# Kernel optimization log

Hardware: AMD Instinct MI355X
Metric: run time of the kernel (lower is better)

Reference implementation:

```python
import jax, jax.numpy as jnp
import numpy as np
import math

V = 32000      # vocab_size
D = 1024       # hidden_dims
T_MAX = 1024   # max_txt_len
L = 4          # n_layers
H = 8          # heads (fixed in CausalMHA)
HD = D // H
B, T = 2, 1024
EPS = 1e-5


def setup_inputs() -> dict:
    key = jax.random.key(0)
    ks = jax.random.split(key, 20)
    s = 0.02
    inp = {
        "x": jax.random.randint(ks[0], (B, T), 0, V, dtype=jnp.int64) if jax.config.read("jax_enable_x64") else jax.random.randint(ks[0], (B, T), 0, V, dtype=jnp.int32),
        "tok_emb": jax.random.normal(ks[1], (V, D), jnp.float32) * s,
        "pos_emb": jax.random.normal(ks[2], (1, T_MAX, D), jnp.float32) * s,
        "ln1_g": jnp.ones((L, D), jnp.float32),
        "ln1_b": jnp.zeros((L, D), jnp.float32),
        "wqkv": jax.random.normal(ks[3], (L, D, 3 * D), jnp.float32) * s,
        "bqkv": jnp.zeros((L, 3 * D), jnp.float32),
        "wo": jax.random.normal(ks[4], (L, D, D), jnp.float32) * s,
        "bo": jnp.zeros((L, D), jnp.float32),
        "ln2_g": jnp.ones((L, D), jnp.float32),
        "ln2_b": jnp.zeros((L, D), jnp.float32),
        "wfc": jax.random.normal(ks[5], (L, D, 4 * D), jnp.float32) * s,   # no bias
        "wfc2": jax.random.normal(ks[6], (L, 4 * D, D), jnp.float32) * s,  # no bias
        "fn_g": jnp.ones((D,), jnp.float32),
        "fn_b": jnp.zeros((D,), jnp.float32),
        "wout": jax.random.normal(ks[7], (D, V), jnp.float32) * s,
        "bout": jnp.zeros((V,), jnp.float32),
    }
    return inp


def _ln(x, g, b):
    mu = jnp.mean(x, axis=-1, keepdims=True)
    var = jnp.var(x, axis=-1, keepdims=True)
    return (x - mu) * jax.lax.rsqrt(var + EPS) * g + b


def _attn(xn, wqkv_l, bqkv_l, wo_l, bo_l):
    Bb, Tt, _ = xn.shape
    qkv = xn @ wqkv_l + bqkv_l                      # [B,T,3D]
    q, k, v = jnp.split(qkv, 3, axis=-1)
    q = q.reshape(Bb, Tt, H, HD)
    k = k.reshape(Bb, Tt, H, HD)
    v = v.reshape(Bb, Tt, H, HD)
    scores = jnp.einsum("bqhd,bkhd->bhqk", q, k) / math.sqrt(HD)
    mask = jnp.triu(jnp.ones((Tt, Tt), bool), k=1)   # True above diagonal
    scores = jnp.where(mask, jnp.float32(-jnp.inf), scores)
    att = jax.nn.softmax(scores, axis=-1)
    out = jnp.einsum("bhqk,bkhd->bqhd", att, v).reshape(Bb, Tt, D)
    return out @ wo_l + bo_l


def reference(x, tok_emb, pos_emb, ln1_g, ln1_b, wqkv, bqkv, wo, bo,
              ln2_g, ln2_b, wfc, wfc2, fn_g, fn_b, wout, bout):
    Tt = x.shape[1]
    h = tok_emb[x] + pos_emb[:, :Tt, :]              # [B,T,D]
    for i in range(L):
        h = h + _attn(_ln(h, ln1_g[i], ln1_b[i]), wqkv[i], bqkv[i], wo[i], bo[i])
        hn = _ln(h, ln2_g[i], ln2_b[i])
        h = h + jax.nn.gelu(hn @ wfc[i], approximate=False) @ wfc2[i]
    h = _ln(h, fn_g, fn_b)
    return h @ wout + bout                           # [B,T,V] logits
```

## Files before the change

kernel.cpp:

```cpp
#include <hip/hip_runtime.h>
#include <math.h>
#include <stdint.h>

#define D_  1024
#define T_  1024
#define H_  8
#define HD_ 128
#define L_  4
#define V_  32000
#define M_  2048

typedef __attribute__((ext_vector_type(4))) float f32x4;
typedef __attribute__((ext_vector_type(4))) short s16x4;
typedef __attribute__((ext_vector_type(8))) short s16x8;
typedef unsigned short u16;

__device__ __forceinline__ u16 f2bf(float f) {
  union { float f; uint32_t u; } c; c.f = f;
  uint32_t r = c.u + 0x7fffu + ((c.u >> 16) & 1u);
  return (u16)(r >> 16);
}
__device__ __forceinline__ float bf2f(u16 h) {
  union { uint32_t u; float f; } c; c.u = ((uint32_t)h) << 16;
  return c.f;
}
__device__ __forceinline__ float gelu_f(float x) {
  return 0.5f * x * (1.0f + erff(x * 0.70710678118654752f));
}

__device__ __forceinline__ void gload16(const u16* g, u16* l) {
  __builtin_amdgcn_global_load_lds(
      (const __attribute__((address_space(1))) void*)(uintptr_t)g,
      (__attribute__((address_space(3))) void*)(uint32_t)(uintptr_t)l,
      16, 0, 0);
}

template<int INF32>
__global__ __launch_bounds__(256)
void convT_kernel(const void* __restrict__ inv, u16* __restrict__ out,
                  int ldin, int ldout, long inZ, long outZ)
{
  __shared__ __align__(16) u16 tile[64][72];
  const int c0 = blockIdx.x << 6, r0 = blockIdx.y << 6;
  const int t = threadIdx.x;
  const int rr = t >> 2, cs = (t & 3) << 4;
  u16 tmp[16];
  if (INF32) {
    const float* in = (const float*)inv + (size_t)blockIdx.z * inZ;
    const float* p = in + (size_t)(r0 + rr) * ldin + c0 + cs;
#pragma unroll
    for (int q = 0; q < 4; ++q) {
      f32x4 v = *(const f32x4*)(p + q * 4);
#pragma unroll
      for (int j = 0; j < 4; ++j) tmp[q * 4 + j] = f2bf(v[j]);
    }
  } else {
    const u16* in = (const u16*)inv + (size_t)blockIdx.z * inZ;
    const u16* p = in + (size_t)(r0 + rr) * ldin + c0 + cs;
    s16x8 v0 = *(const s16x8*)(p);
    s16x8 v1 = *(const s16x8*)(p + 8);
#pragma unroll
    for (int j = 0; j < 8; ++j) { tmp[j] = (u16)v0[j]; tmp[8 + j] = (u16)v1[j]; }
  }
  *(s16x8*)&tile[rr][cs]     = *(const s16x8*)tmp;
  *(s16x8*)&tile[rr][cs + 8] = *(const s16x8*)(tmp + 8);
  __syncthreads();
  const int cr = t >> 2, rs = (t & 3) << 4;
  u16 o[16];
#pragma unroll
  for (int j = 0; j < 16; ++j) o[j] = tile[rs + j][cr];
  u16* op = out + (size_t)blockIdx.z * outZ + (size_t)(c0 + cr) * ldout + r0 + rs;
  *(s16x8*)op       = *(const s16x8*)o;
  *(s16x8*)(op + 8) = *(const s16x8*)(o + 8);
}

template<int TM, int ACT, int BIAS, int OUT>
__global__ __launch_bounds__(256)
void gemm2(const u16* __restrict__ A, const u16* __restrict__ Bw,
           const float* __restrict__ bias, const float* __restrict__ res,
           void* __restrict__ Cv,
           int K, int lda, int ldb, int ldc, float scale)
{
  static_assert(TM == 64 || TM == 128, "tile");
  constexpr int WN  = (TM == 128) ? 2 : 4;
  constexpr int WNW = 128 / WN;
  constexpr int NJ  = WNW / 16;
  constexpr int AR  = TM / 64;

  const int gx = gridDim.x, gy = gridDim.y;
  int flat = blockIdx.y * gx + blockIdx.x;
  const int nwg = gx * gy;
  int swz = (flat & 7) * (nwg >> 3) + (flat >> 3);
  const int bx = swz % gx;
  const int by = swz / gx;

  const int m0 = bx * TM, n0 = by * 128;
  const int ktiles = K >> 5;

  __shared__ __align__(16) u16 As[2][TM * 32];
  __shared__ __align__(16) u16 Bs[2][128 * 32];

  const int tid = threadIdx.x, lane = tid & 63, wave = tid >> 6;
  const int wm = wave / WN, wn = wave % WN;
  const int l15 = lane & 15, l4 = lane >> 4;
  const int srow = lane >> 2, scol = (lane & 3) << 3;

  f32x4 acc[4][NJ];
  const f32x4 z4 = {0.f, 0.f, 0.f, 0.f};
#pragma unroll
  for (int i = 0; i < 4; ++i)
#pragma unroll
    for (int j = 0; j < NJ; ++j) acc[i][j] = z4;

  auto stage = [&](int kt, int buf) {
    const int kc = (kt << 5) + scol;
#pragma unroll
    for (int r = 0; r < AR; ++r) {
      const int row = r * 64 + wave * 16;
      gload16(A + (size_t)(m0 + row + srow) * lda + kc, &As[buf][row * 32]);
    }
#pragma unroll
    for (int r = 0; r < 2; ++r) {
      const int row = r * 64 + wave * 16;
      gload16(Bw + (size_t)(n0 + row + srow) * ldb + kc, &Bs[buf][row * 32]);
    }
  };

  stage(0, 0);
  __syncthreads();

  for (int kt = 0; kt < ktiles; ++kt) {
    const int buf = kt & 1;
    if (kt + 1 < ktiles) stage(kt + 1, buf ^ 1);
    const u16* ap = &As[buf][(wm * 64 + l15) * 32 + (l4 << 3)];
    const u16* bp = &Bs[buf][(wn * WNW + l15) * 32 + (l4 << 3)];
    s16x8 af[4], bf[NJ];
#pragma unroll
    for (int i = 0; i < 4; ++i) af[i] = *(const s16x8*)(ap + i * (16 * 32));
#pragma unroll
    for (int j = 0; j < NJ; ++j) bf[j] = *(const s16x8*)(bp + j * (16 * 32));
#pragma unroll
    for (int i = 0; i < 4; ++i)
#pragma unroll
      for (int j = 0; j < NJ; ++j)
        acc[i][j] = __builtin_amdgcn_mfma_f32_16x16x32_bf16(af[i], bf[j], acc[i][j], 0, 0, 0);
    __syncthreads();
  }

  float* Cf = (float*)Cv;
  u16*   Ch = (u16*)Cv;
#pragma unroll
  for (int i = 0; i < 4; ++i) {
    const int row0 = m0 + wm * 64 + i * 16 + l4 * 4;
#pragma unroll
    for (int j = 0; j < NJ; ++j) {
      const int col = n0 + wn * WNW + j * 16 + l15;
      const float bv = BIAS ? bias[col] : 0.0f;
#pragma unroll
      for (int r = 0; r < 4; ++r) {
        float v = acc[i][j][r] * scale + bv;
        if (ACT) v = gelu_f(v);
        const size_t idx = (size_t)(row0 + r) * ldc + col;
        if (OUT == 0)      Ch[idx] = f2bf(v);
        else if (OUT == 1) Cf[idx] = v;
        else               Cf[idx] = v + res[idx];
      }
    }
  }
}

__global__ __launch_bounds__(256)
void flash_attn(const u16* __restrict__ qkv, const u16* __restrict__ Vt,
                u16* __restrict__ xo)
{
  const int qb = 15 - blockIdx.x;
  const int z  = blockIdx.y;
  const int b  = z >> 3, hh = z & 7;

  __shared__ __align__(16) u16 Ks[64 * 128];
  __shared__ __align__(16) u16 Vs[128 * 64];
  __shared__ __align__(16) u16 Ps[64 * 80];

  const int tid = threadIdx.x, lane = tid & 63, w = tid >> 6;
  const int l15 = lane & 15, l4 = lane >> 4;
  const float iscale = 0.08838834764831845f;

  const int qrow = qb * 64 + w * 16 + l15;
  const u16* qptr = qkv + ((size_t)(b * T_) + qrow) * (3 * D_) + hh * HD_;

  s16x8 bQ[4];
#pragma unroll
  for (int ks = 0; ks < 4; ++ks)
    bQ[ks] = *(const s16x8*)(qptr + ks * 32 + l4 * 8);

  f32x4 O[8];
#pragma unroll
  for (int i = 0; i < 8; ++i) O[i] = {0.f, 0.f, 0.f, 0.f};
  float m_run = -1e30f, l_run = 0.f;

  const int ntiles = qb + 1;
  for (int kt = 0; kt < ntiles; ++kt) {
    __syncthreads();
    {
      const int r = tid >> 2, c = (tid & 3) << 5;
      const u16* src = qkv + ((size_t)(b * T_) + kt * 64 + r) * (3 * D_) + D_ + hh * HD_ + c;
#pragma unroll
      for (int u = 0; u < 4; ++u) {
        s16x8 v = *(const s16x8*)(src + u * 8);
        const int dblk = (c >> 3) + u;
        *(s16x8*)&Ks[r * 128 + ((dblk ^ (r & 7)) << 3)] = v;
      }
      const int d = tid >> 1, kc0 = (tid & 1) << 5;
      const u16* vsrc = Vt + ((size_t)z * HD_ + d) * T_ + kt * 64 + kc0;
#pragma unroll
      for (int u = 0; u < 4; ++u) {
        s16x8 v = *(const s16x8*)(vsrc + u * 8);
        const int kblk = (kc0 >> 3) + u;
        *(s16x8*)&Vs[d * 64 + ((kblk ^ (d & 7)) << 3)] = v;
      }
    }
    __syncthreads();

    f32x4 st[4];
#pragma unroll
    for (int mf = 0; mf < 4; ++mf) st[mf] = {0.f, 0.f, 0.f, 0.f};
#pragma unroll
    for (int ks = 0; ks < 4; ++ks) {
      s16x8 aK[4];
#pragma unroll
      for (int mf = 0; mf < 4; ++mf) {
        const int r = mf * 16 + l15;
        aK[mf] = *(const s16x8*)&Ks[r * 128 + ((((ks << 2) + l4) ^ (r & 7)) << 3)];
      }
#pragma unroll
      for (int mf = 0; mf < 4; ++mf)
        st[mf] = __builtin_amdgcn_mfma_f32_16x16x32_bf16(aK[mf], bQ[ks], st[mf], 0, 0, 0);
    }

    const bool diag = (kt == qb);
    float sv[16];
    float mx = -1e30f;
#pragma unroll
    for (int mf = 0; mf < 4; ++mf)
#pragma unroll
      for (int r = 0; r < 4; ++r) {
        float s = st[mf][r] * iscale;
        if (diag) {
          const int k = kt * 64 + mf * 16 + l4 * 4 + r;
          if (k > qrow) s = -1e30f;
        }
        sv[mf * 4 + r] = s;
        mx = fmaxf(mx, s);
      }
    mx = fmaxf(mx, __shfl_xor(mx, 16));
    mx = fmaxf(mx, __shfl_xor(mx, 32));
    const float m_new = fmaxf(m_run, mx);
    const float sc_old = __expf(m_run - m_new);
    float psum = 0.f;
    u16 pb[16];
#pragma unroll
    for (int j = 0; j < 16; ++j) {
      const float p = __expf(sv[j] - m_new);
      psum += p;
      pb[j] = f2bf(p);
    }
    psum += __shfl_xor(psum, 16);
    psum += __shfl_xor(psum, 32);
    l_run = l_run * sc_old + psum;
    m_run = m_new;

    float scr[4];
#pragma unroll
    for (int r = 0; r < 4; ++r) scr[r] = __shfl(sc_old, l4 * 4 + r);
#pragma unroll
    for (int df = 0; df < 8; ++df)
#pragma unroll
      for (int r = 0; r < 4; ++r) O[df][r] *= scr[r];

    {
      const int row = w * 16 + l15;
#pragma unroll
      for (int j = 0; j < 16; ++j) {
        const int k = (j >> 2) * 16 + l4 * 4 + (j & 3);
        Ps[row * 80 + (((k >> 3) ^ (l15 & 7)) << 3) + (k & 7)] = pb[j];
      }
    }

#pragma unroll
    for (int kc = 0; kc < 2; ++kc) {
      const int prow = w * 16 + l15;
      s16x8 aP = *(const s16x8*)&Ps[prow * 80 + ((((kc << 2) + l4) ^ (l15 & 7)) << 3)];
#pragma unroll
      for (int df = 0; df < 8; ++df) {
        const int d = df * 16 + l15;
        s16x8 bV = *(const s16x8*)&Vs[d * 64 + ((((kc << 2) + l4) ^ (d & 7)) << 3)];
        O[df] = __builtin_amdgcn_mfma_f32_16x16x32_bf16(aP, bV, O[df], 0, 0, 0);
      }
    }
  }

  const float inv_l = 1.0f / l_run;
  float invr[4];
#pragma unroll
  for (int r = 0; r < 4; ++r) invr[r] = __shfl(inv_l, l4 * 4 + r);
#pragma unroll
  for (int df = 0; df < 8; ++df)
#pragma unroll
    for (int r = 0; r < 4; ++r) {
      const int row = qb * 64 + w * 16 + l4 * 4 + r;
      xo[((size_t)(b * T_) + row) * D_ + hh * HD_ + df * 16 + l15] =
          f2bf(O[df][r] * invr[r]);
    }
}

__global__ __launch_bounds__(512, 2)
void gemm8_logits(const u16* __restrict__ A, const u16* __restrict__ Bw,
                  const float* __restrict__ bias, float* __restrict__ C)
{
  int flat = blockIdx.x;
  int swz = (flat & 7) * 125 + (flat >> 3);
  const int bx = swz & 7;
  const int by = swz >> 3;
  const int m0 = bx << 8, n0 = by << 8;

  __shared__ __align__(16) u16 lds[65536];

  const int tid = threadIdx.x, lane = tid & 63, wave = tid >> 6;
  const int wm = wave >> 2, wn = wave & 3;
  const int l15 = lane & 15, l4 = lane >> 4;

  f32x4 acc[8][4];
  const f32x4 z4 = {0.f, 0.f, 0.f, 0.f};
#pragma unroll
  for (int i = 0; i < 8; ++i)
#pragma unroll
    for (int j = 0; j < 4; ++j) acc[i][j] = z4;

  auto stg = [&](const u16* G, int rowbase, int slot, int kt, int kh) {
    if (kt >= 16) return;
#pragma unroll
    for (int r = 0; r < 2; ++r) {
      const int u = r * 512 + (wave << 6) + lane;
      const int rw = u >> 2, ks = u & 3;
      const int ksw = ks ^ ((rw >> 1) & 3);
      const u16* src = G + (size_t)(rowbase + rw) * 1024 + (kt << 6) + (kh << 5) + (ksw << 3);
      gload16(src, &lds[slot + r * 4096 + (wave << 9)]);
    }
  };

  s16x8 af[4], bfr[4];

#define LDA4(bb, kk, mh)                                                      \
  {                                                                           \
    _Pragma("unroll") for (int f = 0; f < 4; ++f) {                           \
      const int rw = wm * 128 + (mh) * 64 + f * 16 + l15;                     \
      af[f] = *(const s16x8*)&lds[(bb) + (kk) * 8192 + rw * 32 +              \
                                  ((l4 ^ ((rw >> 1) & 3)) << 3)];             \
    }                                                                         \
  }
#define LDB4(bb, kk)                                                          \
  {                                                                           \
    _Pragma("unroll") for (int f = 0; f < 4; ++f) {                           \
      const int rn = wn * 64 + f * 16 + l15;                                  \
      bfr[f] = *(const s16x8*)&lds[(bb) + 16384 + (kk) * 8192 + rn * 32 +     \
                                   ((l4 ^ ((rn >> 1) & 3)) << 3)];            \
    }                                                                         \
  }
#define MFMA16(mh)                                                            \
  {                                                                           \
    __builtin_amdgcn_s_barrier();                                             \
    asm volatile("s_waitcnt lgkmcnt(0)" ::: "memory");                        \
    __builtin_amdgcn_sched_barrier(0);                                        \
    __builtin_amdgcn_s_setprio(1);                                            \
    _Pragma("unroll") for (int f = 0; f < 4; ++f)                             \
      _Pragma("unroll") for (int nf = 0; nf < 4; ++nf)                        \
        acc[(mh) * 4 + f][nf] = __builtin_amdgcn_mfma_f32_16x16x32_bf16(      \
            af[f], bfr[nf], acc[(mh) * 4 + f][nf], 0, 0, 0);                  \
    __builtin_amdgcn_s_setprio(0);                                            \
  }
#define BAR() __builtin_amdgcn_s_barrier()
#define VM4() asm volatile("s_waitcnt vmcnt(4)" ::: "memory")

  stg(A,  m0, 0,             0, 0);
  stg(Bw, n0, 16384,         0, 0);
  stg(A,  m0, 8192,          0, 1);
  stg(Bw, n0, 16384 + 8192,  0, 1);
  stg(A,  m0, 32768,         1, 0);
  stg(Bw, n0, 32768 + 16384, 1, 0);
  VM4();
  BAR();

  for (int i = 0; i < 8; ++i) {
    const int t = 2 * i;
    LDA4(0, 0, 0); LDB4(0, 0);
    stg(A, m0, 32768 + 8192, t + 1, 1);
    MFMA16(0); BAR();
    LDA4(0, 0, 1);
    stg(Bw, n0, 32768 + 24576, t + 1, 1);
    MFMA16(1); BAR();
    LDA4(0, 1, 0); LDB4(0, 1);
    stg(A, m0, 0, t + 2, 0);
    MFMA16(0); BAR();
    LDA4(0, 1, 1);
    stg(Bw, n0, 16384, t + 2, 0);
    MFMA16(1); VM4(); BAR();
    LDA4(32768, 0, 0); LDB4(32768, 0);
    stg(A, m0, 8192, t + 2, 1);
    MFMA16(0); BAR();
    LDA4(32768, 0, 1);
    stg(Bw, n0, 16384 + 8192, t + 2, 1);
    MFMA16(1); BAR();
    LDA4(32768, 1, 0); LDB4(32768, 1);
    stg(A, m0, 32768, t + 3, 0);
    MFMA16(0); BAR();
    LDA4(32768, 1, 1);
    stg(Bw, n0, 32768 + 16384, t + 3, 0);
    MFMA16(1); VM4(); BAR();
  }
#undef LDA4
#undef LDB4
#undef MFMA16
#undef BAR
#undef VM4

  float bv[4];
#pragma unroll
  for (int nf = 0; nf < 4; ++nf) bv[nf] = bias[n0 + wn * 64 + nf * 16 + l15];
#pragma unroll
  for (int mf = 0; mf < 8; ++mf) {
    const int row0 = m0 + wm * 128 + mf * 16 + l4 * 4;
#pragma unroll
    for (int nf = 0; nf < 4; ++nf) {
      const int col = n0 + wn * 64 + nf * 16 + l15;
#pragma unroll
      for (int r = 0; r < 4; ++r)
        C[(size_t)(row0 + r) * V_ + col] = acc[mf][nf][r] + bv[nf];
    }
  }
}

__global__ __launch_bounds__(256)
void ln_bf16(const float* __restrict__ x, const float* __restrict__ g,
             const float* __restrict__ b, u16* __restrict__ y)
{
  __shared__ float red[8];
  const int row = blockIdx.x, tid = threadIdx.x;
  f32x4 v = *(const f32x4*)&x[(size_t)row * D_ + tid * 4];
  float s  = v[0] + v[1] + v[2] + v[3];
  float s2 = v[0]*v[0] + v[1]*v[1] + v[2]*v[2] + v[3]*v[3];
#pragma unroll
  for (int off = 32; off > 0; off >>= 1) {
    s  += __shfl_xor(s, off);
    s2 += __shfl_xor(s2, off);
  }
  if ((tid & 63) == 0) { red[tid >> 6] = s; red[4 + (tid >> 6)] = s2; }
  __syncthreads();
  s  = red[0] + red[1] + red[2] + red[3];
  s2 = red[4] + red[5] + red[6] + red[7];
  const float mean = s * (1.0f / D_);
  const float var  = s2 * (1.0f / D_) - mean * mean;
  const float rs   = rsqrtf(var + 1e-5f);
  f32x4 gg = *(const f32x4*)&g[tid * 4];
  f32x4 bb = *(const f32x4*)&b[tid * 4];
  u16 o[4];
#pragma unroll
  for (int j = 0; j < 4; ++j) o[j] = f2bf((v[j] - mean) * rs * gg[j] + bb[j]);
  *(s16x4*)&y[(size_t)row * D_ + tid * 4] = *(const s16x4*)o;
}

__global__ __launch_bounds__(256)
void embed_kernel(const int* __restrict__ x, const float* __restrict__ tok,
                  const float* __restrict__ pos, float* __restrict__ h)
{
  const int row = blockIdx.x, tid = threadIdx.x;
  const int t = row & (T_ - 1);
  const int id = x[row];
  f32x4 a = *(const f32x4*)&tok[(size_t)id * D_ + tid * 4];
  f32x4 p = *(const f32x4*)&pos[(size_t)t * D_ + tid * 4];
  f32x4 o = {a[0] + p[0], a[1] + p[1], a[2] + p[2], a[3] + p[3]};
  *(f32x4*)&h[(size_t)row * D_ + tid * 4] = o;
}

extern "C" void kernel_launch(void* const* d_in, const int* in_sizes, int n_in,
                              void* d_out, int out_size, void* d_ws, size_t ws_size,
                              hipStream_t stream)
{
  (void)in_sizes; (void)n_in; (void)out_size; (void)ws_size;
  const int*   x     = (const int*)  d_in[0];
  const float* tok   = (const float*)d_in[1];
  const float* pos   = (const float*)d_in[2];
  const float* ln1_g = (const float*)d_in[3];
  const float* ln1_b = (const float*)d_in[4];
  const float* wqkv  = (const float*)d_in[5];
  const float* bqkv  = (const float*)d_in[6];
  const float* wo    = (const float*)d_in[7];
  const float* bo    = (const float*)d_in[8];
  const float* ln2_g = (const float*)d_in[9];
  const float* ln2_b = (const float*)d_in[10];
  const float* wfc   = (const float*)d_in[11];
  const float* wfc2  = (const float*)d_in[12];
  const float* fn_g  = (const float*)d_in[13];
  const float* fn_b  = (const float*)d_in[14];
  const float* wout  = (const float*)d_in[15];
  const float* bout  = (const float*)d_in[16];
  float* out = (float*)d_out;

  float* h  = (float*)d_ws;
  u16* xn   = (u16*)(h + (size_t)M_ * D_);
  u16* Wq   = xn  + (size_t)M_ * D_;
  u16* Wo   = Wq  + (size_t)3 * D_ * D_;
  u16* Wf1  = Wo  + (size_t)D_ * D_;
  u16* Wf2  = Wf1 + (size_t)4 * D_ * D_;
  u16* qkv  = Wf2 + (size_t)4 * D_ * D_;
  u16* Vt   = qkv + (size_t)M_ * 3 * D_;
  u16* S    = Vt  + (size_t)2 * T_ * D_;
  u16* WoutT = Wq;

  embed_kernel<<<M_, 256, 0, stream>>>(x, tok, pos, h);

  for (int l = 0; l < L_; ++l) {
    convT_kernel<1><<<dim3(48, 16, 1), 256, 0, stream>>>(
        wqkv + (size_t)l * D_ * 3 * D_, Wq, 3 * D_, D_, 0, 0);
    convT_kernel<1><<<dim3(16, 16, 1), 256, 0, stream>>>(
        wo + (size_t)l * D_ * D_, Wo, D_, D_, 0, 0);
    convT_kernel<1><<<dim3(64, 16, 1), 256, 0, stream>>>(
        wfc + (size_t)l * D_ * 4 * D_, Wf1, 4 * D_, D_, 0, 0);
    convT_kernel<1><<<dim3(16, 64, 1), 256, 0, stream>>>(
        wfc2 + (size_t)l * 4 * D_ * D_, Wf2, D_, 4 * D_, 0, 0);

    ln_bf16<<<M_, 256, 0, stream>>>(h, ln1_g + l * D_, ln1_b + l * D_, xn);
    gemm2<128, 0, 1, 0><<<dim3(16, 24), 256, 0, stream>>>(
        xn, Wq, bqkv + l * 3 * D_, nullptr, qkv, D_, D_, D_, 3 * D_, 1.0f);
    convT_kernel<0><<<dim3(16, 16, 2), 256, 0, stream>>>(
        qkv + 2 * D_, Vt, 3 * D_, T_, (long)T_ * 3 * D_, (long)T_ * D_);
    flash_attn<<<dim3(16, 16), 256, 0, stream>>>(qkv, Vt, xn);
    gemm2<64, 0, 1, 2><<<dim3(32, 8), 256, 0, stream>>>(
        xn, Wo, bo + l * D_, h, h, D_, D_, D_, D_, 1.0f);
    ln_bf16<<<M_, 256, 0, stream>>>(h, ln2_g + l * D_, ln2_b + l * D_, xn);
    gemm2<128, 1, 0, 0><<<dim3(16, 32), 256, 0, stream>>>(
        xn, Wf1, nullptr, nullptr, S, D_, D_, D_, 4 * D_, 1.0f);
    gemm2<64, 0, 0, 2><<<dim3(32, 8), 256, 0, stream>>>(
        S, Wf2, nullptr, h, h, 4 * D_, 4 * D_, 4 * D_, D_, 1.0f);
  }

  ln_bf16<<<M_, 256, 0, stream>>>(h, fn_g, fn_b, xn);
  convT_kernel<1><<<dim3(500, 16, 1), 256, 0, stream>>>(
      wout, WoutT, V_, D_, 0, 0);
  gemm8_logits<<<1000, 512, 0, stream>>>(xn, WoutT, bout, out);
}
```

Baseline: 1.004 ms.

## Route QKV and FC1 GEMMs through 256x256 tile kernel; fuse weight conversions

Generalizes the large-tile 512-thread logits GEMM kernel with templated output type, GELU and optional bias, then uses it for the QKV and FC1 projections instead of the 128x128 gemm2 kernel. It also merges the four per-layer weight transpose/convert launches into a single 3072-block kernel. The larger tiles raise data reuse, and the merged conversion cuts launch count. The risk is that the big-tile grids are small (96 and 128 blocks), which may leave many compute units idle on a 256-CU part.

```diff
diff --git a/kernel.cpp b/kernel.cpp
--- a/kernel.cpp
+++ b/kernel.cpp
@@ -35,32 +35,21 @@
       16, 0, 0);
 }
 
-template<int INF32>
-__global__ __launch_bounds__(256)
-void convT_kernel(const void* __restrict__ inv, u16* __restrict__ out,
-                  int ldin, int ldout, long inZ, long outZ)
-{
-  __shared__ __align__(16) u16 tile[64][72];
-  const int c0 = blockIdx.x << 6, r0 = blockIdx.y << 6;
+__device__ __forceinline__ void convT_f32_tile(const float* __restrict__ in,
+                                               u16* __restrict__ out,
+                                               int ldin, int ldout,
+                                               int c0, int r0,
+                                               u16 (*tile)[72])
+{
   const int t = threadIdx.x;
   const int rr = t >> 2, cs = (t & 3) << 4;
   u16 tmp[16];
-  if (INF32) {
-    const float* in = (const float*)inv + (size_t)blockIdx.z * inZ;
-    const float* p = in + (size_t)(r0 + rr) * ldin + c0 + cs;
-#pragma unroll
-    for (int q = 0; q < 4; ++q) {
-      f32x4 v = *(const f32x4*)(p + q * 4);
-#pragma unroll
-      for (int j = 0; j < 4; ++j) tmp[q * 4 + j] = f2bf(v[j]);
-    }
-  } else {
-    const u16* in = (const u16*)inv + (size_t)blockIdx.z * inZ;
-    const u16* p = in + (size_t)(r0 + rr) * ldin + c0 + cs;
-    s16x8 v0 = *(const s16x8*)(p);
-    s16x8 v1 = *(const s16x8*)(p + 8);
-#pragma unroll
-    for (int j = 0; j < 8; ++j) { tmp[j] = (u16)v0[j]; tmp[8 + j] = (u16)v1[j]; }
+  const float* p = in + (size_t)(r0 + rr) * ldin + c0 + cs;
+#pragma unroll
+  for (int q = 0; q < 4; ++q) {
+    f32x4 v = *(const f32x4*)(p + q * 4);
+#pragma unroll
+    for (int j = 0; j < 4; ++j) tmp[q * 4 + j] = f2bf(v[j]);
   }
   *(s16x8*)&tile[rr][cs]     = *(const s16x8*)tmp;
   *(s16x8*)&tile[rr][cs + 8] = *(const s16x8*)(tmp + 8);
@@ -69,19 +58,70 @@
   u16 o[16];
 #pragma unroll
   for (int j = 0; j < 16; ++j) o[j] = tile[rs + j][cr];
+  u16* op = out + (size_t)(c0 + cr) * ldout + r0 + rs;
+  *(s16x8*)op       = *(const s16x8*)o;
+  *(s16x8*)(op + 8) = *(const s16x8*)(o + 8);
+}
+
+template<int INF32>
+__global__ __launch_bounds__(256)
+void convT_kernel(const void* __restrict__ inv, u16* __restrict__ out,
+                  int ldin, int ldout, long inZ, long outZ)
+{
+  __shared__ __align__(16) u16 tile[64][72];
+  const int c0 = blockIdx.x << 6, r0 = blockIdx.y << 6;
+  if (INF32) {
+    convT_f32_tile((const float*)inv + (size_t)blockIdx.z * inZ,
+                   out + (size_t)blockIdx.z * outZ, ldin, ldout, c0, r0, tile);
+    return;
+  }
+  const int t = threadIdx.x;
+  const int rr = t >> 2, cs = (t & 3) << 4;
+  const u16* in = (const u16*)inv + (size_t)blockIdx.z * inZ;
+  const u16* p = in + (size_t)(r0 + rr) * ldin + c0 + cs;
+  s16x8 v0 = *(const s16x8*)(p);
+  s16x8 v1 = *(const s16x8*)(p + 8);
+  *(s16x8*)&tile[rr][cs]     = v0;
+  *(s16x8*)&tile[rr][cs + 8] = v1;
+  __syncthreads();
+  const int cr = t >> 2, rs = (t & 3) << 4;
+  u16 o[16];
+#pragma unroll
+  for (int j = 0; j < 16; ++j) o[j] = tile[rs + j][cr];
   u16* op = out + (size_t)blockIdx.z * outZ + (size_t)(c0 + cr) * ldout + r0 + rs;
   *(s16x8*)op       = *(const s16x8*)o;
   *(s16x8*)(op + 8) = *(const s16x8*)(o + 8);
 }
 
+__global__ __launch_bounds__(256)
+void conv4_kernel(const float* __restrict__ wqkv_l, const float* __restrict__ wo_l,
+                  const float* __restrict__ wfc_l, const float* __restrict__ wfc2_l,
+                  u16* __restrict__ Wq, u16* __restrict__ Wo,
+                  u16* __restrict__ Wf1, u16* __restrict__ Wf2)
+{
+  __shared__ __align__(16) u16 tile[64][72];
+  int f = blockIdx.x;
+  if (f < 768) {
+    convT_f32_tile(wqkv_l, Wq, 3 * D_, D_, (f % 48) << 6, (f / 48) << 6, tile);
+  } else if (f < 1024) {
+    f -= 768;
+    convT_f32_tile(wo_l, Wo, D_, D_, (f & 15) << 6, (f >> 4) << 6, tile);
+  } else if (f < 2048) {
+    f -= 1024;
+    convT_f32_tile(wfc_l, Wf1, 4 * D_, D_, (f & 63) << 6, (f >> 6) << 6, tile);
+  } else {
+    f -= 2048;
+    convT_f32_tile(wfc2_l, Wf2, D_, 4 * D_, (f & 15) << 6, (f >> 4) << 6, tile);
+  }
+}
+
 template<int TM, int ACT, int BIAS, int OUT>
-__global__ __launch_bounds__(256)
-void gemm2(const u16* __restrict__ A, const u16* __restrict__ Bw,
-           const float* __restrict__ bias, const float* __restrict__ res,
-           void* __restrict__ Cv,
-           int K, int lda, int ldb, int ldc, float scale)
-{
-  static_assert(TM == 64 || TM == 128, "tile");
+__device__ __forceinline__
+void gemm2_body(const u16* __restrict__ A, const u16* __restrict__ Bw,
+                const float* __restrict__ bias, const float* __restrict__ res,
+                void* __restrict__ Cv,
+                int K, int lda, int ldb, int ldc, float scale)
+{
   constexpr int WN  = (TM == 128) ? 2 : 4;
   constexpr int WNW = 128 / WN;
   constexpr int NJ  = WNW / 16;
@@ -170,155 +210,24 @@
 }
 
 __global__ __launch_bounds__(256)
-void flash_attn(const u16* __restrict__ qkv, const u16* __restrict__ Vt,
-                u16* __restrict__ xo)
-{
-  const int qb = 15 - blockIdx.x;
-  const int z  = blockIdx.y;
-  const int b  = z >> 3, hh = z & 7;
-
-  __shared__ __align__(16) u16 Ks[64 * 128];
-  __shared__ __align__(16) u16 Vs[128 * 64];
-  __shared__ __align__(16) u16 Ps[64 * 80];
-
-  const int tid = threadIdx.x, lane = tid & 63, w = tid >> 6;
-  const int l15 = lane & 15, l4 = lane >> 4;
-  const float iscale = 0.08838834764831845f;
-
-  const int qrow = qb * 64 + w * 16 + l15;
-  const u16* qptr = qkv + ((size_t)(b * T_) + qrow) * (3 * D_) + hh * HD_;
-
-  s16x8 bQ[4];
-#pragma unroll
-  for (int ks = 0; ks < 4; ++ks)
-    bQ[ks] = *(const s16x8*)(qptr + ks * 32 + l4 * 8);
-
-  f32x4 O[8];
-#pragma unroll
-  for (int i = 0; i < 8; ++i) O[i] = {0.f, 0.f, 0.f, 0.f};
-  float m_run = -1e30f, l_run = 0.f;
-
-  const int ntiles = qb + 1;
-  for (int kt = 0; kt < ntiles; ++kt) {
-    __syncthreads();
-    {
-      const int r = tid >> 2, c = (tid & 3) << 5;
-      const u16* src = qkv + ((size_t)(b * T_) + kt * 64 + r) * (3 * D_) + D_ + hh * HD_ + c;
-#pragma unroll
-      for (int u = 0; u < 4; ++u) {
-        s16x8 v = *(const s16x8*)(src + u * 8);
-        const int dblk = (c >> 3) + u;
-        *(s16x8*)&Ks[r * 128 + ((dblk ^ (r & 7)) << 3)] = v;
-      }
-      const int d = tid >> 1, kc0 = (tid & 1) << 5;
-      const u16* vsrc = Vt + ((size_t)z * HD_ + d) * T_ + kt * 64 + kc0;
-#pragma unroll
-      for (int u = 0; u < 4; ++u) {
-        s16x8 v = *(const s16x8*)(vsrc + u * 8);
-        const int kblk = (kc0 >> 3) + u;
-        *(s16x8*)&Vs[d * 64 + ((kblk ^ (d & 7)) << 3)] = v;
-      }
-    }
-    __syncthreads();
-
-    f32x4 st[4];
-#pragma unroll
-    for (int mf = 0; mf < 4; ++mf) st[mf] = {0.f, 0.f, 0.f, 0.f};
-#pragma unroll
-    for (int ks = 0; ks < 4; ++ks) {
-      s16x8 aK[4];
-#pragma unroll
-      for (int mf = 0; mf < 4; ++mf) {
-        const int r = mf * 16 + l15;
-        aK[mf] = *(const s16x8*)&Ks[r * 128 + ((((ks << 2) + l4) ^ (r & 7)) << 3)];
-      }
-#pragma unroll
-      for (int mf = 0; mf < 4; ++mf)
-        st[mf] = __builtin_amdgcn_mfma_f32_16x16x32_bf16(aK[mf], bQ[ks], st[mf], 0, 0, 0);
-    }
-
-    const bool diag = (kt == qb);
-    float sv[16];
-    float mx = -1e30f;
-#pragma unroll
-    for (int mf = 0; mf < 4; ++mf)
-#pragma unroll
-      for (int r = 0; r < 4; ++r) {
-        float s = st[mf][r] * iscale;
-        if (diag) {
-          const int k = kt * 64 + mf * 16 + l4 * 4 + r;
-          if (k > qrow) s = -1e30f;
-        }
-        sv[mf * 4 + r] = s;
-        mx = fmaxf(mx, s);
-      }
-    mx = fmaxf(mx, __shfl_xor(mx, 16));
-    mx = fmaxf(mx, __shfl_xor(mx, 32));
-    const float m_new = fmaxf(m_run, mx);
-    const float sc_old = __expf(m_run - m_new);
-    float psum = 0.f;
-    u16 pb[16];
-#pragma unroll
-    for (int j = 0; j < 16; ++j) {
-      const float p = __expf(sv[j] - m_new);
-      psum += p;
-      pb[j] = f2bf(p);
-    }
-    psum += __shfl_xor(psum, 16);
-    psum += __shfl_xor(psum, 32);
-    l_run = l_run * sc_old + psum;
-    m_run = m_new;
-
-    float scr[4];
-#pragma unroll
-    for (int r = 0; r < 4; ++r) scr[r] = __shfl(sc_old, l4 * 4 + r);
-#pragma unroll
-    for (int df = 0; df < 8; ++df)
-#pragma unroll
-      for (int r = 0; r < 4; ++r) O[df][r] *= scr[r];
-
-    {
-      const int row = w * 16 + l15;
-#pragma unroll
-      for (int j = 0; j < 16; ++j) {
-        const int k = (j >> 2) * 16 + l4 * 4 + (j & 3);
-        Ps[row * 80 + (((k >> 3) ^ (l15 & 7)) << 3) + (k & 7)] = pb[j];
-      }
-    }
-
-#pragma unroll
-    for (int kc = 0; kc < 2; ++kc) {
-      const int prow = w * 16 + l15;
-      s16x8 aP = *(const s16x8*)&Ps[prow * 80 + ((((kc << 2) + l4) ^ (l15 & 7)) << 3)];
-#pragma unroll
-      for (int df = 0; df < 8; ++df) {
-        const int d = df * 16 + l15;
-        s16x8 bV = *(const s16x8*)&Vs[d * 64 + ((((kc << 2) + l4) ^ (d & 7)) << 3)];
-        O[df] = __builtin_amdgcn_mfma_f32_16x16x32_bf16(aP, bV, O[df], 0, 0, 0);
-      }
-    }
-  }
-
-  const float inv_l = 1.0f / l_run;
-  float invr[4];
-#pragma unroll
-  for (int r = 0; r < 4; ++r) invr[r] = __shfl(inv_l, l4 * 4 + r);
-#pragma unroll
-  for (int df = 0; df < 8; ++df)
-#pragma unroll
-    for (int r = 0; r < 4; ++r) {
-      const int row = qb * 64 + w * 16 + l4 * 4 + r;
-      xo[((size_t)(b * T_) + row) * D_ + hh * HD_ + df * 16 + l15] =
-          f2bf(O[df][r] * invr[r]);
-    }
-}
-
-__global__ __launch_bounds__(512, 2)
-void gemm8_logits(const u16* __restrict__ A, const u16* __restrict__ Bw,
-                  const float* __restrict__ bias, float* __restrict__ C)
-{
+void gemm_wo(const u16* A, const u16* Bw, const float* bias, const float* res,
+             void* Cv, int K, int lda, int ldb, int ldc, float scale) {
+  gemm2_body<64, 0, 1, 2>(A, Bw, bias, res, Cv, K, lda, ldb, ldc, scale);
+}
+__global__ __launch_bounds__(256)
+void gemm_fc2(const u16* A, const u16* Bw, const float* bias, const float* res,
+              void* Cv, int K, int lda, int ldb, int ldc, float scale) {
+  gemm2_body<64, 0, 0, 2>(A, Bw, bias, res, Cv, K, lda, ldb, ldc, scale);
+}
+
+template<int OUT, int ACT, int BIAS>
+__device__ __forceinline__
+void gemm8_body(const u16* __restrict__ A, const u16* __restrict__ Bw,
+                const float* __restrict__ bias, void* __restrict__ Cv, int ldc)
+{
+  const int cpx = gridDim.x >> 3;
   int flat = blockIdx.x;
-  int swz = (flat & 7) * 125 + (flat >> 3);
+  int swz = (flat & 7) * cpx + (flat >> 3);
   const int bx = swz & 7;
   const int by = swz >> 3;
   const int m0 = bx << 8, n0 = by << 8;
@@ -425,7 +334,10 @@
 
   float bv[4];
 #pragma unroll
-  for (int nf = 0; nf < 4; ++nf) bv[nf] = bias[n0 + wn * 64 + nf * 16 + l15];
+  for (int nf = 0; nf < 4; ++nf)
+    bv[nf] = BIAS ? bias[n0 + wn * 64 + nf * 16 + l15] : 0.0f;
+  float* Cf = (float*)Cv;
+  u16*   Ch = (u16*)Cv;
 #pragma unroll
   for (int mf = 0; mf < 8; ++mf) {
     const int row0 = m0 + wm * 128 + mf * 16 + l4 * 4;
@@ -433,10 +345,172 @@
     for (int nf = 0; nf < 4; ++nf) {
       const int col = n0 + wn * 64 + nf * 16 + l15;
 #pragma unroll
-      for (int r = 0; r < 4; ++r)
-        C[(size_t)(row0 + r) * V_ + col] = acc[mf][nf][r] + bv[nf];
-    }
-  }
+      for (int r = 0; r < 4; ++r) {
+        float v = acc[mf][nf][r] + bv[nf];
+        if (ACT) v = gelu_f(v);
+        const size_t idx = (size_t)(row0 + r) * ldc + col;
+        if (OUT == 0) Ch[idx] = f2bf(v);
+        else          Cf[idx] = v;
+      }
+    }
+  }
+}
+
+__global__ __launch_bounds__(512, 2)
+void gemm8_logits(const u16* A, const u16* Bw, const float* bias, void* Cv, int ldc) {
+  gemm8_body<1, 0, 1>(A, Bw, bias, Cv, ldc);
+}
+__global__ __launch_bounds__(512, 2)
+void gemm8_qkv(const u16* A, const u16* Bw, const float* bias, void* Cv, int ldc) {
+  gemm8_body<0, 0, 1>(A, Bw, bias, Cv, ldc);
+}
+__global__ __launch_bounds__(512, 2)
+void gemm8_fc1(const u16* A, const u16* Bw, const float* bias, void* Cv, int ldc) {
+  gemm8_body<0, 1, 0>(A, Bw, bias, Cv, ldc);
+}
+
+__global__ __launch_bounds__(256)
+void flash_attn(const u16* __restrict__ qkv, const u16* __restrict__ Vt,
+                u16* __restrict__ xo)
+{
+  const int qb = 15 - blockIdx.x;
+  const int z  = blockIdx.y;
+  const int b  = z >> 3, hh = z & 7;
+
+  __shared__ __align__(16) u16 Ks[64 * 128];
+  __shared__ __align__(16) u16 Vs[128 * 64];
+  __shared__ __align__(16) u16 Ps[64 * 80];
+
+  const int tid = threadIdx.x, lane = tid & 63, w = tid >> 6;
+  const int l15 = lane & 15, l4 = lane >> 4;
+  const float iscale = 0.08838834764831845f;
+
+  const int qrow = qb * 64 + w * 16 + l15;
+  const u16* qptr = qkv + ((size_t)(b * T_) + qrow) * (3 * D_) + hh * HD_;
+
+  s16x8 bQ[4];
+#pragma unroll
+  for (int ks = 0; ks < 4; ++ks)
+    bQ[ks] = *(const s16x8*)(qptr + ks * 32 + l4 * 8);
+
+  f32x4 O[8];
+#pragma unroll
+  for (int i = 0; i < 8; ++i) O[i] = {0.f, 0.f, 0.f, 0.f};
+  float m_run = -1e30f, l_run = 0.f;
+
+  const int ntiles = qb + 1;
+  for (int kt = 0; kt < ntiles; ++kt) {
+    __syncthreads();
+    {
+      const int r = tid >> 2, c = (tid & 3) << 5;
+      const u16* src = qkv + ((size_t)(b * T_) + kt * 64 + r) * (3 * D_) + D_ + hh * HD_ + c;
+#pragma unroll
+      for (int u = 0; u < 4; ++u) {
+        s16x8 v = *(const s16x8*)(src + u * 8);
+        const int dblk = (c >> 3) + u;
+        *(s16x8*)&Ks[r * 128 + ((dblk ^ (r & 7)) << 3)] = v;
+      }
+      const int d = tid >> 1, kc0 = (tid & 1) << 5;
+      const u16* vsrc = Vt + ((size_t)z * HD_ + d) * T_ + kt * 64 + kc0;
+#pragma unroll
+      for (int u = 0; u < 4; ++u) {
+        s16x8 v = *(const s16x8*)(vsrc + u * 8);
+        const int kblk = (kc0 >> 3) + u;
+        *(s16x8*)&Vs[d * 64 + ((kblk ^ (d & 7)) << 3)] = v;
+      }
+    }
+    __syncthreads();
+
+    f32x4 st[4];
+#pragma unroll
+    for (int mf = 0; mf < 4; ++mf) st[mf] = {0.f, 0.f, 0.f, 0.f};
+#pragma unroll
+    for (int ks = 0; ks < 4; ++ks) {
+      s16x8 aK[4];
+#pragma unroll
+      for (int mf = 0; mf < 4; ++mf) {
+        const int r = mf * 16 + l15;
+        aK[mf] = *(const s16x8*)&Ks[r * 128 + ((((ks << 2) + l4) ^ (r & 7)) << 3)];
+      }
+#pragma unroll
+      for (int mf = 0; mf < 4; ++mf)
+        st[mf] = __builtin_amdgcn_mfma_f32_16x16x32_bf16(aK[mf], bQ[ks], st[mf], 0, 0, 0);
+    }
+
+    const bool diag = (kt == qb);
+    float sv[16];
+    float mx = -1e30f;
+#pragma unroll
+    for (int mf = 0; mf < 4; ++mf)
+#pragma unroll
+      for (int r = 0; r < 4; ++r) {
+        float s = st[mf][r] * iscale;
+        if (diag) {
+          const int k = kt * 64 + mf * 16 + l4 * 4 + r;
+          if (k > qrow) s = -1e30f;
+        }
+        sv[mf * 4 + r] = s;
+        mx = fmaxf(mx, s);
+      }
+    mx = fmaxf(mx, __shfl_xor(mx, 16));
+    mx = fmaxf(mx, __shfl_xor(mx, 32));
+    const float m_new = fmaxf(m_run, mx);
+    const float sc_old = __expf(m_run - m_new);
+    float psum = 0.f;
+    u16 pb[16];
+#pragma unroll
+    for (int j = 0; j < 16; ++j) {
+      const float p = __expf(sv[j] - m_new);
+      psum += p;
+      pb[j] = f2bf(p);
+    }
+    psum += __shfl_xor(psum, 16);
+    psum += __shfl_xor(psum, 32);
+    l_run = l_run * sc_old + psum;
+    m_run = m_new;
+
+    float scr[4];
+#pragma unroll
+    for (int r = 0; r < 4; ++r) scr[r] = __shfl(sc_old, l4 * 4 + r);
+#pragma unroll
+    for (int df = 0; df < 8; ++df)
+#pragma unroll
+      for (int r = 0; r < 4; ++r) O[df][r] *= scr[r];
+
+    {
+      const int row = w * 16 + l15;
+#pragma unroll
+      for (int j = 0; j < 16; ++j) {
+        const int k = (j >> 2) * 16 + l4 * 4 + (j & 3);
+        Ps[row * 80 + (((k >> 3) ^ (l15 & 7)) << 3) + (k & 7)] = pb[j];
+      }
+    }
+
+#pragma unroll
+    for (int kc = 0; kc < 2; ++kc) {
+      const int prow = w * 16 + l15;
+      s16x8 aP = *(const s16x8*)&Ps[prow * 80 + ((((kc << 2) + l4) ^ (l15 & 7)) << 3)];
+#pragma unroll
+      for (int df = 0; df < 8; ++df) {
+        const int d = df * 16 + l15;
+        s16x8 bV = *(const s16x8*)&Vs[d * 64 + ((((kc << 2) + l4) ^ (d & 7)) << 3)];
+        O[df] = __builtin_amdgcn_mfma_f32_16x16x32_bf16(aP, bV, O[df], 0, 0, 0);
+      }
+    }
+  }
+
+  const float inv_l = 1.0f / l_run;
+  float invr[4];
+#pragma unroll
+  for (int r = 0; r < 4; ++r) invr[r] = __shfl(inv_l, l4 * 4 + r);
+#pragma unroll
+  for (int df = 0; df < 8; ++df)
+#pragma unroll
+    for (int r = 0; r < 4; ++r) {
+      const int row = qb * 64 + w * 16 + l4 * 4 + r;
+      xo[((size_t)(b * T_) + row) * D_ + hh * HD_ + df * 16 + l15] =
+          f2bf(O[df][r] * invr[r]);
+    }
 }
 
 __global__ __launch_bounds__(256)
@@ -519,32 +593,26 @@
   embed_kernel<<<M_, 256, 0, stream>>>(x, tok, pos, h);
 
   for (int l = 0; l < L_; ++l) {
-    convT_kernel<1><<<dim3(48, 16, 1), 256, 0, stream>>>(
-        wqkv + (size_t)l * D_ * 3 * D_, Wq, 3 * D_, D_, 0, 0);
-    convT_kernel<1><<<dim3(16, 16, 1), 256, 0, stream>>>(
-        wo + (size_t)l * D_ * D_, Wo, D_, D_, 0, 0);
-    convT_kernel<1><<<dim3(64, 16, 1), 256, 0, stream>>>(
-        wfc + (size_t)l * D_ * 4 * D_, Wf1, 4 * D_, D_, 0, 0);
-    convT_kernel<1><<<dim3(16, 64, 1), 256, 0, stream>>>(
-        wfc2 + (size_t)l * 4 * D_ * D_, Wf2, D_, 4 * D_, 0, 0);
+    conv4_kernel<<<3072, 256, 0, stream>>>(
+        wqkv + (size_t)l * D_ * 3 * D_, wo + (size_t)l * D_ * D_,
+        wfc + (size_t)l * D_ * 4 * D_, wfc2 + (size_t)l * 4 * D_ * D_,
+        Wq, Wo, Wf1, Wf2);
 
     ln_bf16<<<M_, 256, 0, stream>>>(h, ln1_g + l * D_, ln1_b + l * D_, xn);
-    gemm2<128, 0, 1, 0><<<dim3(16, 24), 256, 0, stream>>>(
-        xn, Wq, bqkv + l * 3 * D_, nullptr, qkv, D_, D_, D_, 3 * D_, 1.0f);
+    gemm8_qkv<<<96, 512, 0, stream>>>(xn, Wq, bqkv + l * 3 * D_, qkv, 3 * D_);
     convT_kernel<0><<<dim3(16, 16, 2), 256, 0, stream>>>(
         qkv + 2 * D_, Vt, 3 * D_, T_, (long)T_ * 3 * D_, (long)T_ * D_);
     flash_attn<<<dim3(16, 16), 256, 0, stream>>>(qkv, Vt, xn);
-    gemm2<64, 0, 1, 2><<<dim3(32, 8), 256, 0, stream>>>(
+    gemm_wo<<<dim3(32, 8), 256, 0, stream>>>(
         xn, Wo, bo + l * D_, h, h, D_, D_, D_, D_, 1.0f);
     ln_bf16<<<M_, 256, 0, stream>>>(h, ln2_g + l * D_, ln2_b + l * D_, xn);
-    gemm2<128, 1, 0, 0><<<dim3(16, 32), 256, 0, stream>>>(
-        xn, Wf1, nullptr, nullptr, S, D_, D_, D_, 4 * D_, 1.0f);
-    gemm2<64, 0, 0, 2><<<dim3(32, 8), 256, 0, stream>>>(
+    gemm8_fc1<<<128, 512, 0, stream>>>(xn, Wf1, nullptr, S, 4 * D_);
+    gemm_fc2<<<dim3(32, 8), 256, 0, stream>>>(
         S, Wf2, nullptr, h, h, 4 * D_, 4 * D_, 4 * D_, D_, 1.0f);
   }
 
   ln_bf16<<<M_, 256, 0, stream>>>(h, fn_g, fn_b, xn);
   convT_kernel<1><<<dim3(500, 16, 1), 256, 0, stream>>>(
       wout, WoutT, V_, D_, 0, 0);
-  gemm8_logits<<<1000, 512, 0, stream>>>(xn, WoutT, bout, out);
-}
+  gemm8_logits<<<1000, 512, 0, stream>>>(xn, WoutT, bout, out, V_);
+}
```

New measurement: 1.059 ms. 5.4% more time.
